# Optimization experiments

Measured on AMD Instinct MI355X. Metric: run time of the kernel, lower is better.

Reference implementation:

```python
import jax, jax.numpy as jnp
import numpy as np

D = 2048      # d_model
H = 8         # n_head
CHUNK = 128   # chunk_size (hard-coded in source)
NORM_GK = 16.0
EPS = 1e-5


def setup_inputs() -> dict:
    key = jax.random.key(0)
    ks = jax.random.split(key, 10)
    s = 0.02
    return {
        "x":    jax.random.normal(ks[0], (4, 2048, D), jnp.float32),
        "Wq":   jax.random.normal(ks[1], (D, D // 2), jnp.float32) * s,
        "Wk":   jax.random.normal(ks[2], (D, D // 2), jnp.float32) * s,
        "Wkg1": jax.random.normal(ks[3], (D, 16), jnp.float32) * s,
        "Wkg2": jax.random.normal(ks[4], (16, D // 2), jnp.float32) * s,
        "bkg2": jnp.zeros((D // 2,), jnp.float32),
        "Wv":   jax.random.normal(ks[5], (D, D), jnp.float32) * s,
        "Wg":   jax.random.normal(ks[6], (D, D), jnp.float32) * s,
        "bg":   jnp.zeros((D,), jnp.float32),
        "Wo":   jax.random.normal(ks[7], (D, D), jnp.float32) * s,
    }


def _chunked_gla(q, k, v, gk):
    """q,k,gk: (b,h,n,c,dk); v: (b,h,n,c,dv).
    Recurrence: S_t = exp(gk_t)[:,None] * S_{t-1} + k_t^T v_t; o_t = q_t S_t."""
    gkc = jnp.cumsum(gk, axis=-2)                      # inclusive cumsum within chunk
    qd = q * jnp.exp(gkc)                              # decayed q for inter-chunk
    kd = k * jnp.exp(gkc[..., -1:, :] - gkc)           # k decayed to chunk end
    # intra-chunk: A_ij = sum_d q_i exp(gkc_i - gkc_j) k_j, j <= i
    A = jnp.einsum('bhnid,bhnjd->bhnij', qd, k * jnp.exp(-gkc))
    c = q.shape[-2]
    mask = jnp.tril(jnp.ones((c, c), dtype=bool))
    o_intra = jnp.einsum('bhnij,bhnjv->bhniv', jnp.where(mask, A, 0.0), v)
    decay_last = jnp.exp(gkc[..., -1, :])              # (b,h,n,dk)

    def step(S, inp):
        qd_c, kd_c, v_c, dl = inp                      # per chunk
        o1 = jnp.einsum('bhcd,bhdv->bhcv', qd_c, S)
        S = dl[..., :, None] * S + jnp.einsum('bhcd,bhcv->bhdv', kd_c, v_c)
        return S, o1

    b, h, n, _, dk = q.shape
    dv = v.shape[-1]
    S0 = jnp.zeros((b, h, dk, dv), q.dtype)
    xs = (jnp.moveaxis(qd, 2, 0), jnp.moveaxis(kd, 2, 0),
          jnp.moveaxis(v, 2, 0), jnp.moveaxis(decay_last, 2, 0))
    _, o_inter = jax.lax.scan(step, S0, xs)
    o_inter = jnp.moveaxis(o_inter, 0, 2)              # (b,h,n,c,dv)
    return o_inter + o_intra


def reference(x, Wq, Wk, Wkg1, Wkg2, bkg2, Wv, Wg, bg, Wo):
    b, T, _ = x.shape
    n = T // CHUNK
    dk = (D // 2) // H
    dv = D // H
    scaling = (D // H) ** -0.5          # source uses key_dim = d_model // n_head

    q = x @ Wq
    k = (x @ Wk) * scaling
    gk = jax.nn.log_sigmoid((x @ Wkg1) @ Wkg2 + bkg2) / NORM_GK
    v = x @ Wv
    g = x @ Wg + bg

    def split(t, hd):  # (b, n*c, h*hd) -> (b,h,n,c,hd)
        return t.reshape(b, n, CHUNK, H, hd).transpose(0, 3, 1, 2, 4)

    o = _chunked_gla(split(q, dk), split(k, dk), split(v, dv), split(gk, dk))
    # group_norm: LayerNorm over last dim, no affine
    mu = o.mean(-1, keepdims=True)
    var = o.var(-1, keepdims=True)
    o = (o - mu) / jnp.sqrt(var + EPS)
    # b h n c d -> b (n c) (h d)
    o = o.transpose(0, 2, 3, 1, 4).reshape(b, T, D)
    o = jax.nn.silu(g) * o
    return o @ Wo
```

## Files before the change

### kernel.cpp

```cpp
#include <hip/hip_runtime.h>
#include <stdint.h>


typedef unsigned short u16;
typedef unsigned int u32;
typedef __bf16 bf16x8 __attribute__((ext_vector_type(8)));
typedef _Float16 f16x8 __attribute__((ext_vector_type(8)));
typedef float f32x4 __attribute__((ext_vector_type(4)));

__device__ __forceinline__ u16 f2bf(float f) {
  u32 u = __float_as_uint(f);
  u32 r = (u + 0x7fffu + ((u >> 16) & 1u)) >> 16;
  return (u16)r;
}
__device__ __forceinline__ float bf2f(u16 s) {
  return __uint_as_float(((u32)s) << 16);
}
__device__ __forceinline__ u16 f2h(float f) {
  _Float16 h = (_Float16)f;
  return __builtin_bit_cast(u16, h);
}
__device__ __forceinline__ float h2f(u16 u) {
  return (float)__builtin_bit_cast(_Float16, u);
}

__device__ __forceinline__ void load_lds16(const void* g, void* l) {
  auto gp = (const __attribute__((address_space(1))) u32*)(uintptr_t)g;
  auto lp = (__attribute__((address_space(3))) u32*)(u32)(uintptr_t)l;
  __builtin_amdgcn_global_load_lds(gp, lp, 16, 0, 0);
}
__device__ __forceinline__ bf16x8 ldf(const u16* p) { return *(const bf16x8*)p; }
__device__ __forceinline__ f16x8 ldh(const u16* p) { return *(const f16x8*)p; }

__device__ __forceinline__ void unpk(uint4 w0, uint4 w1, bf16x8& hi, bf16x8& lo) {
  union U { uint4 u; bf16x8 v; } a, b;
  a.u.x = __builtin_amdgcn_perm(w0.y, w0.x, 0x05040100u);
  a.u.y = __builtin_amdgcn_perm(w0.w, w0.z, 0x05040100u);
  a.u.z = __builtin_amdgcn_perm(w1.y, w1.x, 0x05040100u);
  a.u.w = __builtin_amdgcn_perm(w1.w, w1.z, 0x05040100u);
  b.u.x = __builtin_amdgcn_perm(w0.y, w0.x, 0x07060302u);
  b.u.y = __builtin_amdgcn_perm(w0.w, w0.z, 0x07060302u);
  b.u.z = __builtin_amdgcn_perm(w1.y, w1.x, 0x07060302u);
  b.u.w = __builtin_amdgcn_perm(w1.w, w1.z, 0x07060302u);
  hi = a.v;
  lo = b.v;
}

__global__ __launch_bounds__(256) void tpose_f16(const float* __restrict__ src,
                                                 u16* __restrict__ dst,
                                                 int srcRows, int srcStride,
                                                 float scale) {
  __shared__ float tile[32][33];
  const int tx = threadIdx.x, ty = threadIdx.y;
  const int n0 = blockIdx.x * 32, k0 = blockIdx.y * 32;
#pragma unroll
  for (int j = 0; j < 4; ++j) {
    int k = k0 + ty + j * 8;
    tile[ty + j * 8][tx] = src[(size_t)k * srcStride + n0 + tx] * scale;
  }
  __syncthreads();
#pragma unroll
  for (int j = 0; j < 4; ++j) {
    int n = n0 + ty + j * 8;
    float f = tile[tx][ty + j * 8];
    dst[(size_t)n * srcRows + k0 + tx] = f2h(f);
  }
}

template <int OUTF32>
__global__ __launch_bounds__(256, 2) void gemm_f16(const u16* __restrict__ A,
                                                   const u16* __restrict__ Bt,
                                                   void* __restrict__ C,
                                                   int M, int N, int K) {
  __shared__ u16 As[128 * 32];
  __shared__ u16 Bs[256 * 32];
  const int tid = threadIdx.x;
  const int wave = tid >> 6, lane = tid & 63;
  const int wm = wave >> 1, wn = wave & 1;
  const int qu = lane >> 4, ln = lane & 15;
  const int m0 = blockIdx.y * 128, n0 = blockIdx.x * 256;
  f32x4 acc[4][8] = {};
  for (int kt = 0; kt < K; kt += 32) {
#pragma unroll
    for (int r = 0; r < 2; ++r) {
      const int idx = r * 256 + tid;
      const int row = idx >> 2, chk = idx & 3;
      const int sc = ((chk ^ ((row >> 1) & 3)) << 3);
      load_lds16(A + (size_t)(m0 + row) * K + kt + sc, As + (size_t)idx * 8);
    }
#pragma unroll
    for (int r = 0; r < 4; ++r) {
      const int idx = r * 256 + tid;
      const int row = idx >> 2, chk = idx & 3;
      const int sc = ((chk ^ ((row >> 1) & 3)) << 3);
      load_lds16(Bt + (size_t)(n0 + row) * K + kt + sc, Bs + (size_t)idx * 8);
    }
    __syncthreads();
    f16x8 af[4], bfr[8];
#pragma unroll
    for (int t = 0; t < 4; ++t) {
      const int ia = wm * 64 + t * 16 + ln;
      af[t] = ldh(&As[ia * 32 + ((qu ^ ((ia >> 1) & 3)) << 3)]);
    }
#pragma unroll
    for (int t = 0; t < 8; ++t) {
      const int ib = wn * 128 + t * 16 + ln;
      bfr[t] = ldh(&Bs[ib * 32 + ((qu ^ ((ib >> 1) & 3)) << 3)]);
    }
#pragma unroll
    for (int ti = 0; ti < 4; ++ti)
#pragma unroll
      for (int tj = 0; tj < 8; ++tj)
        acc[ti][tj] = __builtin_amdgcn_mfma_f32_16x16x32_f16(af[ti], bfr[tj], acc[ti][tj], 0, 0, 0);
    __syncthreads();
  }
#pragma unroll
  for (int ti = 0; ti < 4; ++ti)
#pragma unroll
    for (int tj = 0; tj < 8; ++tj) {
      const int rowb = m0 + wm * 64 + ti * 16 + qu * 4;
      const int col = n0 + wn * 128 + tj * 16 + ln;
#pragma unroll
      for (int r = 0; r < 4; ++r) {
        size_t idx = (size_t)(rowb + r) * N + col;
        if (OUTF32) ((float*)C)[idx] = acc[ti][tj][r];
        else        ((u16*)C)[idx] = f2bf(acc[ti][tj][r]);
      }
    }
}

__global__ __launch_bounds__(256) void xg1_gemm(const float* __restrict__ x,
                                                const float* __restrict__ W1,
                                                float* __restrict__ xg1,
                                                u16* __restrict__ xf) {
  __shared__ float xs[32][40];
  __shared__ float ws2[32][16];
  const int tid = threadIdx.x;
  const int r0 = blockIdx.x * 32;
  const int col = tid & 15, rsub = tid >> 4;
  float acc[2] = {0.f, 0.f};
  for (int kt = 0; kt < 2048; kt += 32) {
    {
      int row = tid >> 3, kk = (tid & 7) << 2;
      float4 f4 = *(const float4*)&x[(size_t)(r0 + row) * 2048 + kt + kk];
      *(float4*)&xs[row][kk] = f4;
      ushort4 hq;
      hq.x = f2h(f4.x); hq.y = f2h(f4.y); hq.z = f2h(f4.z); hq.w = f2h(f4.w);
      *(ushort4*)&xf[(size_t)(r0 + row) * 2048 + kt + kk] = hq;
    }
#pragma unroll
    for (int j = 0; j < 2; ++j) {
      int c = j * 256 + tid;
      ws2[c >> 4][c & 15] = W1[(size_t)(kt + (c >> 4)) * 16 + (c & 15)];
    }
    __syncthreads();
#pragma unroll
    for (int kk = 0; kk < 32; ++kk) {
      float wv = ws2[kk][col];
      acc[0] += xs[rsub][kk] * wv;
      acc[1] += xs[rsub + 16][kk] * wv;
    }
    __syncthreads();
  }
  xg1[(size_t)(r0 + rsub) * 16 + col] = acc[0];
  xg1[(size_t)(r0 + rsub + 16) * 16 + col] = acc[1];
}

__global__ __launch_bounds__(256) void gla_decor(float* __restrict__ QK,
                                                 const float* __restrict__ xg1,
                                                 const float* __restrict__ W2,
                                                 const float* __restrict__ b2,
                                                 float* __restrict__ dl) {
  __shared__ float xg1s[128][16];
  const int tid = threadIdx.x;
  const int bi = blockIdx.x;
  const int b = bi >> 7, n = (bi >> 3) & 15, g = bi & 7;
  const int t0 = b * 2048 + n * 128;
  const bool isK = tid >= 128;
  const int ci = tid & 127;
  const int col = g * 128 + ci;
  u32* base = (u32*)QK + (size_t)t0 * 2048 + (isK ? 1024 : 0) + col;
  float w2r[16];
#pragma unroll
  for (int k = 0; k < 16; ++k) w2r[k] = W2[k * 1024 + col];
  const float b2r = b2[col];
  for (int e = tid; e < 2048; e += 256)
    xg1s[e >> 4][e & 15] = xg1[(size_t)(t0 + (e >> 4)) * 16 + (e & 15)];
  __syncthreads();
  float acc = 0.f;
  const float sgn = isK ? -1.f : 1.f;
  for (int s = 0; s < 128; s += 16) {
    float qv[16];
#pragma unroll
    for (int j = 0; j < 16; ++j) qv[j] = __uint_as_float(base[(size_t)(s + j) * 2048]);
    u32 ov[16];
#pragma unroll
    for (int j = 0; j < 16; ++j) {
      float z = b2r;
#pragma unroll
      for (int kk = 0; kk < 16; ++kk) z += xg1s[s + j][kk] * w2r[kk];
      float gk = (fminf(z, 0.f) - log1pf(expf(-fabsf(z)))) * 0.0625f;
      acc += gk;
      float e = expf(sgn * acc);
      float v = qv[j] * e;
      u16 h = f2bf(v);
      u16 l = f2bf(v - bf2f(h));
      ov[j] = (u32)h | ((u32)l << 16);
    }
#pragma unroll
    for (int j = 0; j < 16; ++j) base[(size_t)(s + j) * 2048] = ov[j];
  }
  if (isK) dl[((size_t)(b * 8 + g) * 16 + n) * 128 + ci] = expf(acc);
}

__global__ __launch_bounds__(256) void gla_intra(const u16* __restrict__ QKu,
                                                 const u16* __restrict__ V,
                                                 u16* __restrict__ Oh) {
  __shared__ u16 pool[39936];
  const int tid = threadIdx.x;
  const int bi = blockIdx.x;
  const int n = bi & 15, h = (bi >> 4) & 7, b = bi >> 7;
  const int t0 = b * 2048 + n * 128;
  const int wave = tid >> 6, lane = tid & 63;
  const int wm = wave >> 1, wn = wave & 1;
  const int qu = lane >> 4, ln = lane & 15;
  const int srow = tid >> 3, schk = tid & 7;
  const int sc = ((schk ^ (srow & 7)) << 3);
  u16* Qi = pool;
  u16* Ki = pool + 8192;
  u16* Amh = pool;
  u16* Aml = pool + 16384;
  u16* VTs = pool + 32768;
  const bool skipQuad = (wm == 0 && wn == 1);
  f32x4 acc[4][4] = {};
  for (int kt = 0; kt < 128; kt += 32) {
#pragma unroll
    for (int r = 0; r < 4; ++r) {
      const int row = srow + r * 32;
      const size_t gb = (size_t)(t0 + row) * 4096 + h * 256 + 2 * kt + sc;
      load_lds16(QKu + gb,        Qi + (r * 32 + wave * 8) * 64);
      load_lds16(QKu + gb + 2048, Ki + (r * 32 + wave * 8) * 64);
    }
    __syncthreads();
    if (!skipQuad) {
      bf16x8 ah[4], al[4], bh[4], bl[4];
#pragma unroll
      for (int t = 0; t < 4; ++t) {
        const int i = wm * 64 + t * 16 + ln;
        const u16* pQ = &Qi[i * 64];
        uint4 w0 = *(const uint4*)&pQ[((2 * qu) ^ (i & 7)) << 3];
        uint4 w1 = *(const uint4*)&pQ[((2 * qu + 1) ^ (i & 7)) << 3];
        unpk(w0, w1, ah[t], al[t]);
        const int j = wn * 64 + t * 16 + ln;
        const u16* pK = &Ki[j * 64];
        uint4 y0 = *(const uint4*)&pK[((2 * qu) ^ (j & 7)) << 3];
        uint4 y1 = *(const uint4*)&pK[((2 * qu + 1) ^ (j & 7)) << 3];
        unpk(y0, y1, bh[t], bl[t]);
      }
      const bool diag = (wm == wn);
#pragma unroll
      for (int ti = 0; ti < 4; ++ti)
#pragma unroll
        for (int tj = 0; tj < 4; ++tj) {
          if (diag && tj > ti) continue;
          acc[ti][tj] = __builtin_amdgcn_mfma_f32_16x16x32_bf16(ah[ti], bh[tj], acc[ti][tj], 0, 0, 0);
          acc[ti][tj] = __builtin_amdgcn_mfma_f32_16x16x32_bf16(ah[ti], bl[tj], acc[ti][tj], 0, 0, 0);
          acc[ti][tj] = __builtin_amdgcn_mfma_f32_16x16x32_bf16(al[ti], bh[tj], acc[ti][tj], 0, 0, 0);
        }
    }
    __syncthreads();
  }
#pragma unroll
  for (int ti = 0; ti < 4; ++ti)
#pragma unroll
    for (int tj = 0; tj < 4; ++tj) {
      const int ib = wm * 64 + ti * 16 + qu * 4;
      const int j = wn * 64 + tj * 16 + ln;
#pragma unroll
      for (int r = 0; r < 4; ++r) {
        const int i = ib + r;
        float v = (j <= i) ? acc[ti][tj][r] : 0.f;
        u16 hi = f2bf(v);
        const int idx = i * 128 + (j ^ ((i & 15) << 3));
        Amh[idx] = hi;
        Aml[idx] = f2bf(v - bf2f(hi));
      }
    }
  for (int half = 0; half < 2; ++half) {
    f32x4 acc2[4][4] = {};
    for (int kt = 0; kt < 128; kt += 32) {
      __syncthreads();
      {
        const int j = tid & 31, dvg = tid >> 5;
#pragma unroll
        for (int rr = 0; rr < 2; ++rr) {
          const int dg = dvg + rr * 8;
          uint4 pv = *(const uint4*)(V + (size_t)(t0 + kt + j) * 2048 + h * 256 + half * 128 + dg * 8);
          u16* dst = VTs + (dg * 8) * 56 + j;
          dst[0]      = (u16)pv.x; dst[56]      = (u16)(pv.x >> 16);
          dst[2 * 56] = (u16)pv.y; dst[3 * 56]  = (u16)(pv.y >> 16);
          dst[4 * 56] = (u16)pv.z; dst[5 * 56]  = (u16)(pv.z >> 16);
          dst[6 * 56] = (u16)pv.w; dst[7 * 56]  = (u16)(pv.w >> 16);
        }
      }
      __syncthreads();
      bf16x8 amh[4], aml[4], bv[4];
#pragma unroll
      for (int t = 0; t < 4; ++t) {
        if (kt <= wm * 64 + t * 16 + 15) {
          const int i = wm * 64 + t * 16 + ln;
          const int cof = (kt + qu * 8) ^ ((i & 15) << 3);
          amh[t] = ldf(&Amh[i * 128 + cof]);
          aml[t] = ldf(&Aml[i * 128 + cof]);
        }
        bv[t] = ldf(&VTs[(wn * 64 + t * 16 + ln) * 56 + qu * 8]);
      }
#pragma unroll
      for (int ti = 0; ti < 4; ++ti) {
        if (kt > wm * 64 + ti * 16 + 15) continue;
#pragma unroll
        for (int tj = 0; tj < 4; ++tj) {
          acc2[ti][tj] = __builtin_amdgcn_mfma_f32_16x16x32_bf16(amh[ti], bv[tj], acc2[ti][tj], 0, 0, 0);
          acc2[ti][tj] = __builtin_amdgcn_mfma_f32_16x16x32_bf16(aml[ti], bv[tj], acc2[ti][tj], 0, 0, 0);
        }
      }
    }
#pragma unroll
    for (int ti = 0; ti < 4; ++ti)
#pragma unroll
      for (int tj = 0; tj < 4; ++tj)
#pragma unroll
        for (int r = 0; r < 4; ++r) {
          const int i = wm * 64 + ti * 16 + qu * 4 + r;
          const int col = half * 128 + wn * 64 + tj * 16 + ln;
          Oh[(size_t)(t0 + i) * 2048 + h * 256 + col] = f2h(acc2[ti][tj][r]);
        }
  }
}

__global__ __launch_bounds__(256) void gla_w(const u16* __restrict__ QKu,
                                             u16* __restrict__ V) {
  __shared__ u16 KTh[128 * 40];
  __shared__ u16 KTl[128 * 40];
  __shared__ u16 VT[256 * 40];
  const int tid = threadIdx.x;
  const int bi = blockIdx.x;
  const int c = bi & 15, h = (bi >> 4) & 7, b = bi >> 7;
  const int t0 = b * 2048 + c * 128;
  const int wave = tid >> 6, lane = tid & 63;
  const int wm = wave >> 1, wn = wave & 1;
  const int qu = lane >> 4, ln = lane & 15;
  const int t = tid & 31, dg0 = tid >> 5;
  f32x4 acc[4][8] = {};
  for (int kt = 0; kt < 128; kt += 32) {
#pragma unroll
    for (int rr = 0; rr < 2; ++rr) {
      const int dg = dg0 + rr * 8;
      const size_t gb = (size_t)(t0 + kt + t) * 4096 + 2048 + h * 256 + dg * 16;
      uint4 w0 = *(const uint4*)(QKu + gb);
      uint4 w1 = *(const uint4*)(QKu + gb + 8);
      u16* dh = KTh + (dg * 8) * 40 + t;
      u16* dL = KTl + (dg * 8) * 40 + t;
      dh[0]      = (u16)w0.x; dL[0]      = (u16)(w0.x >> 16);
      dh[40]     = (u16)w0.y; dL[40]     = (u16)(w0.y >> 16);
      dh[2 * 40] = (u16)w0.z; dL[2 * 40] = (u16)(w0.z >> 16);
      dh[3 * 40] = (u16)w0.w; dL[3 * 40] = (u16)(w0.w >> 16);
      dh[4 * 40] = (u16)w1.x; dL[4 * 40] = (u16)(w1.x >> 16);
      dh[5 * 40] = (u16)w1.y; dL[5 * 40] = (u16)(w1.y >> 16);
      dh[6 * 40] = (u16)w1.z; dL[6 * 40] = (u16)(w1.z >> 16);
      dh[7 * 40] = (u16)w1.w; dL[7 * 40] = (u16)(w1.w >> 16);
    }
#pragma unroll
    for (int rr = 0; rr < 4; ++rr) {
      const int dvg = dg0 + rr * 8;
      uint4 pv = *(const uint4*)(V + (size_t)(t0 + kt + t) * 2048 + h * 256 + dvg * 8);
      u16* dst = VT + (dvg * 8) * 40 + t;
      dst[0]      = (u16)pv.x; dst[40]     = (u16)(pv.x >> 16);
      dst[2 * 40] = (u16)pv.y; dst[3 * 40] = (u16)(pv.y >> 16);
      dst[4 * 40] = (u16)pv.z; dst[5 * 40] = (u16)(pv.z >> 16);
      dst[6 * 40] = (u16)pv.w; dst[7 * 40] = (u16)(pv.w >> 16);
    }
    __syncthreads();
    bf16x8 kh[4], kl[4], bv[8];
#pragma unroll
    for (int ti = 0; ti < 4; ++ti) {
      const int d = wm * 64 + ti * 16 + ln;
      kh[ti] = ldf(&KTh[d * 40 + qu * 8]);
      kl[ti] = ldf(&KTl[d * 40 + qu * 8]);
    }
#pragma unroll
    for (int tj = 0; tj < 8; ++tj)
      bv[tj] = ldf(&VT[(wn * 128 + tj * 16 + ln) * 40 + qu * 8]);
#pragma unroll
    for (int ti = 0; ti < 4; ++ti)
#pragma unroll
      for (int tj = 0; tj < 8; ++tj) {
        acc[ti][tj] = __builtin_amdgcn_mfma_f32_16x16x32_bf16(kh[ti], bv[tj], acc[ti][tj], 0, 0, 0);
        acc[ti][tj] = __builtin_amdgcn_mfma_f32_16x16x32_bf16(kl[ti], bv[tj], acc[ti][tj], 0, 0, 0);
      }
    __syncthreads();
  }
#pragma unroll
  for (int ti = 0; ti < 4; ++ti)
#pragma unroll
    for (int tj = 0; tj < 8; ++tj)
#pragma unroll
      for (int r = 0; r < 4; ++r) {
        const int d = wm * 64 + ti * 16 + qu * 4 + r;
        const int dv = wn * 128 + tj * 16 + ln;
        V[(size_t)(t0 + d) * 2048 + h * 256 + dv] = f2h(acc[ti][tj][r]);
      }
}

__global__ __launch_bounds__(256) void gla_scan(const u16* __restrict__ QKu,
                                                const u16* __restrict__ W,
                                                const float* __restrict__ dl,
                                                u16* __restrict__ Oh) {
  __shared__ float STf[32 * 128];
  __shared__ u16 STh[32 * 136];
  __shared__ u16 STl[32 * 136];
  __shared__ u16 Qi2[128 * 256];
  __shared__ float dls[128];
  const int tid = threadIdx.x;
  const int bi = blockIdx.x;
  const int sl = bi >> 5, g = bi & 31, b = g >> 3, h = g & 7;
  const int wave = tid >> 6, lane = tid & 63;
  const int qu = lane >> 4, ln = lane & 15;
  const int bh16 = (b * 8 + h) * 16;
  for (int e = tid; e < 4096; e += 256) STf[e] = 0.f;
  for (int c = 0; c < 16; ++c) {
    const int t0 = b * 2048 + c * 128;
    if (tid < 128) dls[tid] = dl[(size_t)(bh16 + c) * 128 + tid];
    uint2 wreg[2][2];
#pragma unroll
    for (int tj = 0; tj < 2; ++tj)
#pragma unroll
      for (int ti = 0; ti < 2; ++ti) {
        const int d = wave * 32 + tj * 16 + ln;
        const int dv = sl * 32 + ti * 16 + qu * 4;
        wreg[tj][ti] = *(const uint2*)(W + (size_t)(t0 + d) * 2048 + h * 256 + dv);
      }
    __syncthreads();
    if (c > 0) {
      for (int e = tid; e < 4096; e += 256) {
        const int row = e >> 7, col = e & 127;
        float v = STf[e];
        u16 hi = f2bf(v);
        STh[row * 136 + col] = hi;
        STl[row * 136 + col] = f2bf(v - bf2f(hi));
      }
#pragma unroll
      for (int r = 0; r < 16; ++r) {
        const int idx = r * 256 + tid;
        const int row = idx >> 5, chk = idx & 31;
        load_lds16(QKu + (size_t)(t0 + row) * 4096 + h * 256 + ((chk ^ (row & 7)) << 3),
                   Qi2 + (size_t)idx * 8);
      }
      __syncthreads();
      f32x4 aco[2][2] = {};
#pragma unroll
      for (int kt = 0; kt < 4; ++kt) {
        bf16x8 qh[2], ql[2], sh[2], slo[2];
#pragma unroll
        for (int t = 0; t < 2; ++t) {
          const int ar = wave * 32 + t * 16 + ln;
          const u16* pQ = &Qi2[ar * 256];
          uint4 w0 = *(const uint4*)&pQ[((kt * 8 + 2 * qu) ^ (ar & 7)) << 3];
          uint4 w1 = *(const uint4*)&pQ[((kt * 8 + 2 * qu + 1) ^ (ar & 7)) << 3];
          unpk(w0, w1, qh[t], ql[t]);
          const int br = t * 16 + ln;
          sh[t]  = ldf(&STh[br * 136 + kt * 32 + qu * 8]);
          slo[t] = ldf(&STl[br * 136 + kt * 32 + qu * 8]);
        }
#pragma unroll
        for (int ti = 0; ti < 2; ++ti)
#pragma unroll
          for (int tj = 0; tj < 2; ++tj) {
            aco[ti][tj] = __builtin_amdgcn_mfma_f32_16x16x32_bf16(qh[ti], sh[tj], aco[ti][tj], 0, 0, 0);
            aco[ti][tj] = __builtin_amdgcn_mfma_f32_16x16x32_bf16(qh[ti], slo[tj], aco[ti][tj], 0, 0, 0);
            aco[ti][tj] = __builtin_amdgcn_mfma_f32_16x16x32_bf16(ql[ti], sh[tj], aco[ti][tj], 0, 0, 0);
          }
      }
#pragma unroll
      for (int ti = 0; ti < 2; ++ti)
#pragma unroll
        for (int tj = 0; tj < 2; ++tj)
#pragma unroll
          for (int r = 0; r < 4; ++r) {
            const int i = wave * 32 + ti * 16 + qu * 4 + r;
            const int dv = tj * 16 + ln;
            u16* p = Oh + (size_t)(t0 + i) * 2048 + h * 256 + sl * 32 + dv;
            *p = f2h(h2f(*p) + aco[ti][tj][r]);
          }
    }
#pragma unroll
    for (int tj = 0; tj < 2; ++tj)
#pragma unroll
      for (int ti = 0; ti < 2; ++ti) {
        const int d = wave * 32 + tj * 16 + ln;
#pragma unroll
        for (int r = 0; r < 4; ++r) {
          const int dv = ti * 16 + qu * 4 + r;
          const u32 wu = (r & 2) ? wreg[tj][ti].y : wreg[tj][ti].x;
          const float wv = h2f((u16)((r & 1) ? (wu >> 16) : (wu & 0xffffu)));
          const int e = dv * 128 + d;
          STf[e] = dls[d] * (STf[e] + wv);
        }
      }
    __syncthreads();
  }
}

__global__ __launch_bounds__(256) void ln_gate(const u16* __restrict__ O,
                                               const u16* __restrict__ G,
                                               const float* __restrict__ bg,
                                               u16* __restrict__ OG) {
  const int tglob = blockIdx.x;
  const int tid = threadIdx.x;
  const int c0 = tid << 3;
  const size_t base = (size_t)tglob * 2048 + c0;
  ushort4 oa = *(const ushort4*)&O[base];
  ushort4 ob = *(const ushort4*)&O[base + 4];
  float f0 = h2f(oa.x), f1 = h2f(oa.y), f2 = h2f(oa.z), f3 = h2f(oa.w);
  float f4 = h2f(ob.x), f5 = h2f(ob.y), f6 = h2f(ob.z), f7 = h2f(ob.w);
  float s = f0 + f1 + f2 + f3 + f4 + f5 + f6 + f7;
  float ss = f0 * f0 + f1 * f1 + f2 * f2 + f3 * f3 + f4 * f4 + f5 * f5 + f6 * f6 + f7 * f7;
#pragma unroll
  for (int off = 1; off <= 16; off <<= 1) {
    s += __shfl_xor(s, off, 64);
    ss += __shfl_xor(ss, off, 64);
  }
  const float mean = s * (1.f / 256.f);
  const float rstd = rsqrtf(ss * (1.f / 256.f) - mean * mean + 1e-5f);
  ushort4 ga = *(const ushort4*)&G[base];
  ushort4 gb4 = *(const ushort4*)&G[base + 4];
  float4 bga = *(const float4*)&bg[c0];
  float4 bgb = *(const float4*)&bg[c0 + 4];
  auto one = [&](float ov, u16 gu, float bgv) -> u16 {
    float gg = bf2f(gu) + bgv;
    return f2h((ov - mean) * rstd * (gg / (1.f + expf(-gg))));
  };
  ushort4 ra, rb;
  ra.x = one(f0, ga.x, bga.x);  ra.y = one(f1, ga.y, bga.y);
  ra.z = one(f2, ga.z, bga.z);  ra.w = one(f3, ga.w, bga.w);
  rb.x = one(f4, gb4.x, bgb.x); rb.y = one(f5, gb4.y, bgb.y);
  rb.z = one(f6, gb4.z, bgb.z); rb.w = one(f7, gb4.w, bgb.w);
  *(ushort4*)&OG[base] = ra;
  *(ushort4*)&OG[base + 4] = rb;
}

extern "C" void kernel_launch(void* const* d_in, const int* in_sizes, int n_in,
                              void* d_out, int out_size, void* d_ws, size_t ws_size,
                              hipStream_t stream) {
  (void)in_sizes; (void)n_in; (void)out_size;
  if (ws_size < 117964800ull) return;

  const float* x    = (const float*)d_in[0];
  const float* Wq   = (const float*)d_in[1];
  const float* Wk   = (const float*)d_in[2];
  const float* Wkg1 = (const float*)d_in[3];
  const float* Wkg2 = (const float*)d_in[4];
  const float* bkg2 = (const float*)d_in[5];
  const float* Wv   = (const float*)d_in[6];
  const float* Wg   = (const float*)d_in[7];
  const float* bg   = (const float*)d_in[8];
  const float* Wo   = (const float*)d_in[9];

  char* ws = (char*)d_ws;
  float* QK  = (float*)(ws + 0);
  u16*   QKu = (u16*)QK;
  u16*   V   = (u16*)(ws + 67108864);
  u16*   Wt  = (u16*)(ws + 100663296);
  float* xg1 = (float*)(ws + 117440512);
  float* dl  = (float*)(ws + 109051904);
  u16*   OG  = (u16*)(ws + 0);

  u16* xf = (u16*)d_out;
  u16* Oh = (u16*)d_out;
  u16* G  = (u16*)d_out + 16777216;

  dim3 tb(32, 8);

  xg1_gemm<<<dim3(256), dim3(256), 0, stream>>>(x, Wkg1, xg1, xf);

  tpose_f16<<<dim3(32, 64), tb, 0, stream>>>(Wq, Wt,               2048, 1024, 1.0f);
  tpose_f16<<<dim3(32, 64), tb, 0, stream>>>(Wk, Wt + 1024 * 2048, 2048, 1024, 0.0625f);
  gemm_f16<1><<<dim3(8, 64), dim3(256), 0, stream>>>(xf, Wt, (void*)QK, 8192, 2048, 2048);

  tpose_f16<<<dim3(64, 64), tb, 0, stream>>>(Wv, Wt, 2048, 2048, 1.0f);
  gemm_f16<0><<<dim3(8, 64), dim3(256), 0, stream>>>(xf, Wt, (void*)V, 8192, 2048, 2048);

  tpose_f16<<<dim3(64, 64), tb, 0, stream>>>(Wg, Wt, 2048, 2048, 1.0f);
  gemm_f16<0><<<dim3(8, 64), dim3(256), 0, stream>>>(xf, Wt, (void*)G, 8192, 2048, 2048);

  gla_decor<<<dim3(512), dim3(256), 0, stream>>>(QK, xg1, Wkg2, bkg2, dl);
  gla_intra<<<dim3(512), dim3(256), 0, stream>>>(QKu, V, Oh);
  gla_w<<<dim3(512), dim3(256), 0, stream>>>(QKu, V);
  gla_scan<<<dim3(256), dim3(256), 0, stream>>>(QKu, V, dl, Oh);
  ln_gate<<<dim3(8192), dim3(256), 0, stream>>>(Oh, G, bg, OG);

  tpose_f16<<<dim3(64, 64), tb, 0, stream>>>(Wo, Wt, 2048, 2048, 1.0f);
  gemm_f16<1><<<dim3(8, 64), dim3(256), 0, stream>>>(OG, Wt, d_out, 8192, 2048, 2048);
}
```

Before: 808.1 us.

## Split x conversion and gate projection into split-K kernels for parallelism

The fused x→f16 conversion plus x@Wkg1 kernel ran only 256 blocks, each looping serially over K=2048. It is replaced by three kernels. A streaming conversion kernel writes the f16 copy of x. A split-K kernel with 1024 blocks computes 16 partial products over 128-wide K slices into a scratch buffer aliased on the weight-transpose region. A reduction kernel then sums the partials. This targets low occupancy and latency in the gate projection, at the cost of reading x twice and extra partial-sum traffic.

```diff
diff --git a/kernel.cpp b/kernel.cpp
--- a/kernel.cpp
+++ b/kernel.cpp
@@ -44,6 +44,70 @@
   b.u.w = __builtin_amdgcn_perm(w1.w, w1.z, 0x07060302u);
   hi = a.v;
   lo = b.v;
+}
+
+__global__ __launch_bounds__(256) void xcvt(const float* __restrict__ x,
+                                            u16* __restrict__ xf) {
+  const size_t i = ((size_t)blockIdx.x * 256 + threadIdx.x) * 8;
+  float4 a = *(const float4*)&x[i];
+  float4 b = *(const float4*)&x[i + 4];
+  ushort4 h0, h1;
+  h0.x = f2h(a.x); h0.y = f2h(a.y); h0.z = f2h(a.z); h0.w = f2h(a.w);
+  h1.x = f2h(b.x); h1.y = f2h(b.y); h1.z = f2h(b.z); h1.w = f2h(b.w);
+  *(ushort4*)&xf[i] = h0;
+  *(ushort4*)&xf[i + 4] = h1;
+}
+
+__global__ __launch_bounds__(256) void xg1p(const float* __restrict__ x,
+                                            const float* __restrict__ W1,
+                                            float* __restrict__ P) {
+  __shared__ float xs[128][132];
+  __shared__ float w1t[16][128];
+  const int tid = threadIdx.x;
+  const int rb = blockIdx.x >> 4, kb = blockIdx.x & 15;
+  const int r0 = rb * 128, k0 = kb * 128;
+#pragma unroll
+  for (int i = 0; i < 16; ++i) {
+    int e = i * 256 + tid;
+    int row = e >> 5, kq = e & 31;
+    *(float4*)&xs[row][kq * 4] = *(const float4*)&x[(size_t)(r0 + row) * 2048 + k0 + kq * 4];
+  }
+#pragma unroll
+  for (int i = 0; i < 8; ++i) {
+    int e = i * 256 + tid;
+    int col = e >> 7, kk = e & 127;
+    w1t[col][kk] = W1[(size_t)(k0 + kk) * 16 + col];
+  }
+  __syncthreads();
+  const int col = tid & 15, rsub = tid >> 4;
+  float acc[8] = {};
+  for (int kc = 0; kc < 128; kc += 16) {
+    float w[16];
+#pragma unroll
+    for (int i = 0; i < 4; ++i)
+      *(float4*)&w[i * 4] = *(const float4*)&w1t[col][kc + i * 4];
+#pragma unroll
+    for (int j = 0; j < 8; ++j) {
+      const int row = j * 16 + rsub;
+#pragma unroll
+      for (int kk = 0; kk < 16; kk += 4) {
+        float4 xv = *(const float4*)&xs[row][kc + kk];
+        acc[j] += xv.x * w[kk] + xv.y * w[kk + 1] + xv.z * w[kk + 2] + xv.w * w[kk + 3];
+      }
+    }
+  }
+#pragma unroll
+  for (int j = 0; j < 8; ++j)
+    P[((size_t)kb * 8192 + r0 + j * 16 + rsub) * 16 + col] = acc[j];
+}
+
+__global__ __launch_bounds__(256) void xg1r(const float* __restrict__ P,
+                                            float* __restrict__ xg1) {
+  const size_t i = (size_t)blockIdx.x * 256 + threadIdx.x;
+  float s = 0.f;
+#pragma unroll
+  for (int kb = 0; kb < 16; ++kb) s += P[(size_t)kb * 131072 + i];
+  xg1[i] = s;
 }
 
 __global__ __launch_bounds__(256) void tpose_f16(const float* __restrict__ src,
@@ -127,43 +191,6 @@
         else        ((u16*)C)[idx] = f2bf(acc[ti][tj][r]);
       }
     }
-}
-
-__global__ __launch_bounds__(256) void xg1_gemm(const float* __restrict__ x,
-                                                const float* __restrict__ W1,
-                                                float* __restrict__ xg1,
-                                                u16* __restrict__ xf) {
-  __shared__ float xs[32][40];
-  __shared__ float ws2[32][16];
-  const int tid = threadIdx.x;
-  const int r0 = blockIdx.x * 32;
-  const int col = tid & 15, rsub = tid >> 4;
-  float acc[2] = {0.f, 0.f};
-  for (int kt = 0; kt < 2048; kt += 32) {
-    {
-      int row = tid >> 3, kk = (tid & 7) << 2;
-      float4 f4 = *(const float4*)&x[(size_t)(r0 + row) * 2048 + kt + kk];
-      *(float4*)&xs[row][kk] = f4;
-      ushort4 hq;
-      hq.x = f2h(f4.x); hq.y = f2h(f4.y); hq.z = f2h(f4.z); hq.w = f2h(f4.w);
-      *(ushort4*)&xf[(size_t)(r0 + row) * 2048 + kt + kk] = hq;
-    }
-#pragma unroll
-    for (int j = 0; j < 2; ++j) {
-      int c = j * 256 + tid;
-      ws2[c >> 4][c & 15] = W1[(size_t)(kt + (c >> 4)) * 16 + (c & 15)];
-    }
-    __syncthreads();
-#pragma unroll
-    for (int kk = 0; kk < 32; ++kk) {
-      float wv = ws2[kk][col];
-      acc[0] += xs[rsub][kk] * wv;
-      acc[1] += xs[rsub + 16][kk] * wv;
-    }
-    __syncthreads();
-  }
-  xg1[(size_t)(r0 + rsub) * 16 + col] = acc[0];
-  xg1[(size_t)(r0 + rsub + 16) * 16 + col] = acc[1];
 }
 
 __global__ __launch_bounds__(256) void gla_decor(float* __restrict__ QK,
@@ -571,6 +598,7 @@
   u16*   QKu = (u16*)QK;
   u16*   V   = (u16*)(ws + 67108864);
   u16*   Wt  = (u16*)(ws + 100663296);
+  float* P   = (float*)(ws + 100663296);
   float* xg1 = (float*)(ws + 117440512);
   float* dl  = (float*)(ws + 109051904);
   u16*   OG  = (u16*)(ws + 0);
@@ -581,7 +609,9 @@
 
   dim3 tb(32, 8);
 
-  xg1_gemm<<<dim3(256), dim3(256), 0, stream>>>(x, Wkg1, xg1, xf);
+  xcvt<<<dim3(8192), dim3(256), 0, stream>>>(x, xf);
+  xg1p<<<dim3(1024), dim3(256), 0, stream>>>(x, Wkg1, P);
+  xg1r<<<dim3(512), dim3(256), 0, stream>>>(P, xg1);
 
   tpose_f16<<<dim3(32, 64), tb, 0, stream>>>(Wq, Wt,               2048, 1024, 1.0f);
   tpose_f16<<<dim3(32, 64), tb, 0, stream>>>(Wk, Wt + 1024 * 2048, 2048, 1024, 0.0625f);
```

New measurement: 776.9 us. -3.9%, faster.
